# Kernel optimization log

Measured on AMD Instinct MI355X. Metric: run time of the kernel, lower is better.

## Reference

```python
import jax, jax.numpy as jnp
import numpy as np

N_NODES = 50000
N_EDGES = 800000
IN_DIM = 128
OUT_DIM = 128
NUM_RELS = 100
NUM_BASES = 4


def setup_inputs() -> dict:
    key = jax.random.key(0)
    ks = jax.random.split(key, 8)
    h = jax.random.normal(ks[0], (N_NODES, IN_DIM), dtype=jnp.float32)
    norm = jax.random.uniform(ks[1], (N_NODES, 1), dtype=jnp.float32)
    src = jax.random.randint(ks[2], (N_EDGES,), 0, N_NODES, dtype=jnp.int32)
    dst = jax.random.randint(ks[3], (N_EDGES,), 0, N_NODES, dtype=jnp.int32)
    rel_type = jax.random.randint(ks[4], (N_EDGES,), 0, NUM_RELS, dtype=jnp.int32)
    basis_weights = jax.random.normal(ks[5], (NUM_BASES, IN_DIM, OUT_DIM), dtype=jnp.float32) * (2.0 / np.sqrt(IN_DIM + OUT_DIM))
    coefficients = jax.random.normal(ks[6], (NUM_RELS, NUM_BASES), dtype=jnp.float32) * (1.0 / np.sqrt(NUM_RELS + NUM_BASES))
    loop_weight = jax.random.normal(ks[7], (IN_DIM, OUT_DIM), dtype=jnp.float32) * (2.0 / np.sqrt(IN_DIM + OUT_DIM))
    return {
        'h': h, 'norm': norm, 'src': src, 'dst': dst, 'rel_type': rel_type,
        'basis_weights': basis_weights, 'coefficients': coefficients,
        'loop_weight': loop_weight,
    }


def reference(h, norm, src, dst, rel_type, basis_weights, coefficients, loop_weight):
    # h: (N, in), norm: (N, 1), src/dst/rel_type: (E,)
    # basis_weights: (B, in, out), coefficients: (R, B), loop_weight: (in, out)
    n_nodes = h.shape[0]
    num_bases = basis_weights.shape[0]

    # self-loop message (dropout=0 -> identity)
    loop_message = h @ loop_weight  # (N, out)

    # W[r] = sum_b coeff[r, b] * basis[b]; per-edge msg_e = h[src_e] @ W[rel_e].
    # Reassociated: project nodes by each basis once, then mix per edge by
    # the relation coefficients -- identical math, avoids the (E, in, out)
    # gathered weight tensor of the original per-edge bmm.
    hb = jnp.einsum('ni,bio->bno', h, basis_weights)  # (B, N, out)
    c_e = coefficients[rel_type]  # (E, B)
    msg = c_e[:, 0, None] * hb[0][src]
    for b in range(1, num_bases):  # small fixed basis count
        msg = msg + c_e[:, b, None] * hb[b][src]  # (E, out)

    # scatter-sum aggregation to destination nodes, then norm scaling
    agg = jax.ops.segment_sum(msg, dst, num_segments=n_nodes)  # (N, out)
    node_repr = agg * norm  # _apply_func
    node_repr = node_repr + loop_message  # self-loop (bias=None)
    return jax.nn.relu(node_repr)  # activation
```

## Files before the change

kernel.cpp:

```cpp
#include <hip/hip_runtime.h>

typedef short bf16x8 __attribute__((ext_vector_type(8)));
typedef float floatx4 __attribute__((ext_vector_type(4)));
typedef float floatx2 __attribute__((ext_vector_type(2)));

typedef const __attribute__((address_space(1))) void* gas_ptr;
typedef __attribute__((address_space(3))) void* las_ptr;

#define EPB  4096
#define MAXB 6144

__device__ __forceinline__ unsigned short f2bf(float f) {
    unsigned int u = __float_as_uint(f);
    unsigned int r = u + 0x7fffu + ((u >> 16) & 1u);
    return (unsigned short)(r >> 16);
}

__device__ __forceinline__ void stage16(const void* g, void* lbase, int lane) {
#if __has_builtin(__builtin_amdgcn_global_load_lds)
    __builtin_amdgcn_global_load_lds((gas_ptr)g, (las_ptr)lbase, 16, 0, 0);
#else
    *(float4*)((char*)lbase + lane * 16) = *(const float4*)g;
#endif
}

__global__ __launch_bounds__(1024) void prep_all(
    const float* __restrict__ h, unsigned short* __restrict__ hbf, int nconv8,
    const int* __restrict__ dst, int* __restrict__ gh, int E, int nB, int nblkH,
    const float* __restrict__ basis, const float* __restrict__ loopw,
    unsigned short* __restrict__ WT2, int nb_conv)
{
    __shared__ int lh[256];
    const int b = blockIdx.x;
    const int t = threadIdx.x;
    if (b < nb_conv) {
        int idx = b * 1024 + t;
        if (idx < nconv8) {
            const float4 v0 = *(const float4*)(h + (size_t)idx * 8);
            const float4 v1 = *(const float4*)(h + (size_t)idx * 8 + 4);
            uint4 p;
            p.x = (unsigned int)f2bf(v0.x) | ((unsigned int)f2bf(v0.y) << 16);
            p.y = (unsigned int)f2bf(v0.z) | ((unsigned int)f2bf(v0.w) << 16);
            p.z = (unsigned int)f2bf(v1.x) | ((unsigned int)f2bf(v1.y) << 16);
            p.w = (unsigned int)f2bf(v1.z) | ((unsigned int)f2bf(v1.w) << 16);
            *(uint4*)(hbf + (size_t)idx * 8) = p;
        }
    } else if (b < nb_conv + nblkH) {
        const int blk = b - nb_conv;
        if (t < 256) lh[t] = 0;
        __syncthreads();
        const int cbase = blk * EPB;
#pragma unroll
        for (int j = 0; j < EPB / 1024; ++j) {
            int e = cbase + j * 1024 + t;
            if (e < E) atomicAdd(&lh[dst[e] >> 8], 1);
        }
        __syncthreads();
        if (t < nB) gh[(size_t)t * nblkH + blk] = lh[t];
    } else {
        int c = b - nb_conv - nblkH;
        if (t < 640) {
            float v;
            if (t < 512) v = basis[(size_t)t * 128 + c];
            else         v = loopw[(size_t)(t - 512) * 128 + c];
            WT2[(size_t)c * 640 + t] = f2bf(v);
        }
    }
}

__global__ __launch_bounds__(256) void scan1(
    const int* __restrict__ in, int* __restrict__ bsum, int M)
{
    __shared__ int s[256];
    int i = blockIdx.x * 256 + threadIdx.x;
    int t = threadIdx.x;
    s[t] = (i < M) ? in[i] : 0;
    __syncthreads();
    for (int o = 128; o > 0; o >>= 1) {
        if (t < o) s[t] += s[t + o];
        __syncthreads();
    }
    if (t == 0) bsum[blockIdx.x] = s[0];
}

__global__ __launch_bounds__(256) void scan_final(
    const int* __restrict__ in, const int* __restrict__ bsum,
    int* __restrict__ out, int M)
{
    __shared__ int s[256];
    __shared__ int sb[256];
    int t = threadIdx.x;
    int i = blockIdx.x * 256 + t;
    sb[t] = (t < (int)blockIdx.x) ? bsum[t] : 0;
    int v = (i < M) ? in[i] : 0;
    s[t] = v;
    __syncthreads();
    for (int o = 128; o > 0; o >>= 1) {
        if (t < o) sb[t] += sb[t + o];
        __syncthreads();
    }
    for (int o = 1; o < 256; o <<= 1) {
        int x = (t >= o) ? s[t - o] : 0;
        __syncthreads();
        s[t] += x;
        __syncthreads();
    }
    if (i < M) out[i] = s[t] - v + sb[0];
}

__global__ __launch_bounds__(1024) void scatter_bkt(
    const int* __restrict__ dst, const int* __restrict__ src,
    const int* __restrict__ rel, const int* __restrict__ sgh,
    unsigned int* __restrict__ tmp, int E, int nB, int nblkH)
{
    __shared__ int cur[256];
    const int blk = blockIdx.x;
    const int t = threadIdx.x;
    if (t < nB) cur[t] = sgh[(size_t)t * nblkH + blk];
    __syncthreads();
    const int cbase = blk * EPB;
#pragma unroll
    for (int j = 0; j < EPB / 1024; ++j) {
        int e = cbase + j * 1024 + t;
        if (e < E) {
            int d = dst[e];
            int slot = atomicAdd(&cur[d >> 8], 1);
            tmp[slot] = (unsigned int)src[e] | ((unsigned int)rel[e] << 16)
                      | ((unsigned int)(d & 255) << 23);
        }
    }
}

__global__ __launch_bounds__(1024) void bucket_sort(
    const unsigned int* __restrict__ tmp, const int* __restrict__ sgh,
    unsigned int* __restrict__ sedge, int* __restrict__ rowptr,
    int E, int N, int nB, int nblkH)
{
    __shared__ unsigned int eb[MAXB];
    __shared__ int hh[256], ss[256], cur[256];
    const int b = blockIdx.x;
    const int t = threadIdx.x;
    const int brow = sgh[(size_t)b * nblkH];
    const int next = (b + 1 < nB) ? sgh[(size_t)(b + 1) * nblkH] : E;
    int n = next - brow;
    if (n > MAXB) n = MAXB;
    if (t < 256) hh[t] = 0;
    __syncthreads();
    for (int i = t; i < n; i += 1024) {
        unsigned int v = tmp[brow + i];
        eb[i] = v;
        atomicAdd(&hh[(v >> 23) & 255], 1);
    }
    __syncthreads();
    int v = 0;
    if (t < 256) { v = hh[t]; ss[t] = v; }
    __syncthreads();
    for (int o = 1; o < 256; o <<= 1) {
        int x = 0;
        if (t < 256 && t >= o) x = ss[t - o];
        __syncthreads();
        if (t < 256) ss[t] += x;
        __syncthreads();
    }
    if (t < 256) {
        const int excl = ss[t] - v;
        const int idx = b * 256 + t;
        if (idx <= N) rowptr[idx] = brow + excl;
        cur[t] = excl;
    }
    __syncthreads();
    for (int i = t; i < n; i += 1024) {
        unsigned int e = eb[i];
        int slot = atomicAdd(&cur[(e >> 23) & 255], 1);
        sedge[brow + slot] = ((e & 0xFFFFu) << 8) | (((e >> 16) & 0x7Fu) << 25);
    }
}

__global__ __launch_bounds__(256, 8) void aggregate_pre(
    const unsigned short* __restrict__ hbf,
    const int* __restrict__ rowptr,
    const unsigned int* __restrict__ sedge,
    const float* __restrict__ coeff,
    const float* __restrict__ norm,
    unsigned short* __restrict__ A2, int N, int R)
{
    __shared__ float scoef[512];
    for (int i = threadIdx.x; i < R * 4; i += 256) scoef[i] = coeff[i];
    __syncthreads();

    const int wave = threadIdx.x >> 6;
    const int lane = threadIdx.x & 63;
    const int d = blockIdx.x * 4 + wave;
    if (d >= N) return;
    int i = rowptr[d];
    const int end = rowptr[d + 1];

    const char* hbase = (const char*)hbf + lane * 4;

    floatx2 a0 = {0.f, 0.f}, a1 = {0.f, 0.f}, a2 = {0.f, 0.f}, a3 = {0.f, 0.f};

#define EDGE_LOAD(v, u) \
    unsigned int u = *(const unsigned int*)(hbase + ((v) & 0x00FFFF00u));
#define EDGE_MATH(v, u) { \
    const float4 c = *(const float4*)((const char*)scoef + (((v) >> 25) << 4)); \
    floatx2 hp; \
    hp[0] = __uint_as_float((u) << 16); \
    hp[1] = __uint_as_float((u) & 0xFFFF0000u); \
    a0 = __builtin_elementwise_fma((floatx2){c.x, c.x}, hp, a0); \
    a1 = __builtin_elementwise_fma((floatx2){c.y, c.y}, hp, a1); \
    a2 = __builtin_elementwise_fma((floatx2){c.z, c.z}, hp, a2); \
    a3 = __builtin_elementwise_fma((floatx2){c.w, c.w}, hp, a3); }

    while (i < end && (i & 3)) {
        unsigned int v = sedge[i];
        EDGE_LOAD(v, u)
        EDGE_MATH(v, u)
        ++i;
    }
    for (; i + 16 <= end; i += 16) {
        uint4 e0 = *(const uint4*)(sedge + i);
        uint4 e1 = *(const uint4*)(sedge + i + 4);
        uint4 e2 = *(const uint4*)(sedge + i + 8);
        uint4 e3 = *(const uint4*)(sedge + i + 12);
        EDGE_LOAD(e0.x, u0)  EDGE_LOAD(e0.y, u1)  EDGE_LOAD(e0.z, u2)  EDGE_LOAD(e0.w, u3)
        EDGE_LOAD(e1.x, u4)  EDGE_LOAD(e1.y, u5)  EDGE_LOAD(e1.z, u6)  EDGE_LOAD(e1.w, u7)
        EDGE_LOAD(e2.x, u8)  EDGE_LOAD(e2.y, u9)  EDGE_LOAD(e2.z, u10) EDGE_LOAD(e2.w, u11)
        EDGE_LOAD(e3.x, u12) EDGE_LOAD(e3.y, u13) EDGE_LOAD(e3.z, u14) EDGE_LOAD(e3.w, u15)
        EDGE_MATH(e0.x, u0)  EDGE_MATH(e0.y, u1)  EDGE_MATH(e0.z, u2)  EDGE_MATH(e0.w, u3)
        EDGE_MATH(e1.x, u4)  EDGE_MATH(e1.y, u5)  EDGE_MATH(e1.z, u6)  EDGE_MATH(e1.w, u7)
        EDGE_MATH(e2.x, u8)  EDGE_MATH(e2.y, u9)  EDGE_MATH(e2.z, u10) EDGE_MATH(e2.w, u11)
        EDGE_MATH(e3.x, u12) EDGE_MATH(e3.y, u13) EDGE_MATH(e3.z, u14) EDGE_MATH(e3.w, u15)
    }
    for (; i + 8 <= end; i += 8) {
        uint4 e0 = *(const uint4*)(sedge + i);
        uint4 e1 = *(const uint4*)(sedge + i + 4);
        EDGE_LOAD(e0.x, u0) EDGE_LOAD(e0.y, u1) EDGE_LOAD(e0.z, u2) EDGE_LOAD(e0.w, u3)
        EDGE_LOAD(e1.x, u4) EDGE_LOAD(e1.y, u5) EDGE_LOAD(e1.z, u6) EDGE_LOAD(e1.w, u7)
        EDGE_MATH(e0.x, u0) EDGE_MATH(e0.y, u1) EDGE_MATH(e0.z, u2) EDGE_MATH(e0.w, u3)
        EDGE_MATH(e1.x, u4) EDGE_MATH(e1.y, u5) EDGE_MATH(e1.z, u6) EDGE_MATH(e1.w, u7)
    }
    for (; i + 4 <= end; i += 4) {
        uint4 e0 = *(const uint4*)(sedge + i);
        EDGE_LOAD(e0.x, u0) EDGE_LOAD(e0.y, u1) EDGE_LOAD(e0.z, u2) EDGE_LOAD(e0.w, u3)
        EDGE_MATH(e0.x, u0) EDGE_MATH(e0.y, u1) EDGE_MATH(e0.z, u2) EDGE_MATH(e0.w, u3)
    }
    for (; i < end; ++i) {
        unsigned int v = sedge[i];
        EDGE_LOAD(v, u)
        EDGE_MATH(v, u)
    }
#undef EDGE_LOAD
#undef EDGE_MATH

    const float nm = norm[d];
    unsigned short* row = A2 + (size_t)d * 512 + lane * 2;
    *(unsigned int*)(row)       = (unsigned int)f2bf(a0[0] * nm) | ((unsigned int)f2bf(a0[1] * nm) << 16);
    *(unsigned int*)(row + 128) = (unsigned int)f2bf(a1[0] * nm) | ((unsigned int)f2bf(a1[1] * nm) << 16);
    *(unsigned int*)(row + 256) = (unsigned int)f2bf(a2[0] * nm) | ((unsigned int)f2bf(a2[1] * nm) << 16);
    *(unsigned int*)(row + 384) = (unsigned int)f2bf(a3[0] * nm) | ((unsigned int)f2bf(a3[1] * nm) << 16);
}

__global__ __launch_bounds__(256) void final_gemm(
    const unsigned short* __restrict__ A2,
    const unsigned short* __restrict__ hbf,
    const unsigned short* __restrict__ WT2,
    float* __restrict__ out, int N)
{
    __shared__ char sA[16384];
    __shared__ char sB[16384];
    const int t = threadIdx.x;
    const int w = t >> 6;
    const int lane = t & 63;
    const int quad = lane >> 4;
    const int low  = lane & 15;
    const int wr = w >> 1, wc = w & 1;
    const int m0 = blockIdx.x * 128;

    floatx4 acc[4][4];
#pragma unroll
    for (int mt = 0; mt < 4; ++mt)
#pragma unroll
        for (int nt = 0; nt < 4; ++nt) acc[mt][nt] = (floatx4){0.f, 0.f, 0.f, 0.f};

    for (int it = 0; it < 10; ++it) {
        const int k0 = it * 64;
#pragma unroll
        for (int i = 0; i < 4; ++i) {
            const int slot = i * 256 + t;
            const int kc  = slot >> 7;
            const int idx = slot & 127;
            int grow = m0 + idx;
            if (grow >= N) grow = N - 1;
            const unsigned short* gA = (k0 < 512)
                ? A2  + (size_t)grow * 512 + k0 + kc * 8
                : hbf + (size_t)grow * 128 + (k0 - 512) + kc * 8;
            const unsigned short* gB = WT2 + (size_t)idx * 640 + k0 + kc * 8;
            stage16(gA, sA + (size_t)(i * 256 + w * 64) * 16, lane);
            stage16(gB, sB + (size_t)(i * 256 + w * 64) * 16, lane);
        }
        __syncthreads();

#pragma unroll
        for (int ks = 0; ks < 2; ++ks) {
            bf16x8 af[4], bfr[4];
#pragma unroll
            for (int mt = 0; mt < 4; ++mt)
                af[mt] = *(const bf16x8*)(sA + (size_t)(((ks * 4 + quad) << 7) + wr * 64 + mt * 16 + low) * 16);
#pragma unroll
            for (int nt = 0; nt < 4; ++nt)
                bfr[nt] = *(const bf16x8*)(sB + (size_t)(((ks * 4 + quad) << 7) + wc * 64 + nt * 16 + low) * 16);
#pragma unroll
            for (int mt = 0; mt < 4; ++mt)
#pragma unroll
                for (int nt = 0; nt < 4; ++nt)
                    acc[mt][nt] = __builtin_amdgcn_mfma_f32_16x16x32_bf16(af[mt], bfr[nt], acc[mt][nt], 0, 0, 0);
        }
        __syncthreads();
    }

#pragma unroll
    for (int mt = 0; mt < 4; ++mt) {
#pragma unroll
        for (int nt = 0; nt < 4; ++nt) {
            const int c = wc * 64 + nt * 16 + low;
#pragma unroll
            for (int r = 0; r < 4; ++r) {
                int rr = m0 + wr * 64 + mt * 16 + quad * 4 + r;
                if (rr < N) out[(size_t)rr * 128 + c] = fmaxf(acc[mt][nt][r], 0.f);
            }
        }
    }
}

extern "C" void kernel_launch(void* const* d_in, const int* in_sizes, int n_in,
                              void* d_out, int out_size, void* d_ws, size_t ws_size,
                              hipStream_t stream)
{
    const float* h     = (const float*)d_in[0];
    const float* norm  = (const float*)d_in[1];
    const int*   src   = (const int*)d_in[2];
    const int*   dst   = (const int*)d_in[3];
    const int*   rel   = (const int*)d_in[4];
    const float* basis = (const float*)d_in[5];
    const float* coeff = (const float*)d_in[6];
    const float* loopw = (const float*)d_in[7];
    float* out = (float*)d_out;

    const int N = in_sizes[1];
    const int E = in_sizes[2];
    const int R = in_sizes[6] / 4;

    const int nB    = (N + 255) >> 8;
    const int nblkH = (E + EPB - 1) / EPB;
    const int M     = nB * nblkH;
    const int NBs   = (M + 255) / 256;

    char* ws = (char*)d_ws;
    size_t off = 0;
    auto walloc = [&](size_t bytes) -> char* {
        char* p = ws + off;
        off = (off + bytes + 255) & ~(size_t)255;
        return p;
    };
    unsigned short* A2     = (unsigned short*)walloc((size_t)N * 512 * 2);
    unsigned short* hbf    = (unsigned short*)walloc((size_t)N * 128 * 2);
    unsigned short* WT2    = (unsigned short*)walloc(128 * 640 * 2);
    int*            rowptr = (int*)walloc((size_t)(N + 1) * 4);
    int*            bsum   = (int*)walloc((size_t)NBs * 4);
    int*            gh     = (int*)walloc((size_t)M * 4);
    int*            sgh    = (int*)walloc((size_t)M * 4);
    unsigned int*   tmp    = (unsigned int*)walloc((size_t)E * 4);
    unsigned int*   sedge  = (unsigned int*)walloc((size_t)E * 4);

    const int nconv8  = N * 16;
    const int nb_conv = (nconv8 + 1023) / 1024;

    prep_all<<<nb_conv + nblkH + 128, 1024, 0, stream>>>(
        h, hbf, nconv8, dst, gh, E, nB, nblkH, basis, loopw, WT2, nb_conv);
    scan1<<<NBs, 256, 0, stream>>>(gh, bsum, M);
    scan_final<<<NBs, 256, 0, stream>>>(gh, bsum, sgh, M);
    scatter_bkt<<<nblkH, 1024, 0, stream>>>(dst, src, rel, sgh, tmp, E, nB, nblkH);
    bucket_sort<<<nB, 1024, 0, stream>>>(tmp, sgh, sedge, rowptr, E, N, nB, nblkH);
    aggregate_pre<<<(N + 3) / 4, 256, 0, stream>>>(hbf, rowptr, sedge, coeff, norm, A2, N, R);
    final_gemm<<<(N + 127) / 128, 256, 0, stream>>>(A2, hbf, WT2, out, N);
}
```

Baseline: 189.9 us.

## Fuse edge bucketing into prep kernel using global atomic bucket reservations

```diff
diff --git a/kernel.cpp b/kernel.cpp
--- a/kernel.cpp
+++ b/kernel.cpp
@@ -26,11 +26,13 @@
 
 __global__ __launch_bounds__(1024) void prep_all(
     const float* __restrict__ h, unsigned short* __restrict__ hbf, int nconv8,
-    const int* __restrict__ dst, int* __restrict__ gh, int E, int nB, int nblkH,
+    const int* __restrict__ dst, const int* __restrict__ src,
+    const int* __restrict__ rel, int* __restrict__ bcnt,
+    unsigned int* __restrict__ tmp, int E, int nB, int nblkH,
     const float* __restrict__ basis, const float* __restrict__ loopw,
     unsigned short* __restrict__ WT2, int nb_conv)
 {
-    __shared__ int lh[256];
+    __shared__ int lh[256], cur[256];
     const int b = blockIdx.x;
     const int t = threadIdx.x;
     if (b < nb_conv) {
@@ -50,13 +52,33 @@
         if (t < 256) lh[t] = 0;
         __syncthreads();
         const int cbase = blk * EPB;
+        int dd[EPB / 1024];
 #pragma unroll
         for (int j = 0; j < EPB / 1024; ++j) {
             int e = cbase + j * 1024 + t;
-            if (e < E) atomicAdd(&lh[dst[e] >> 8], 1);
-        }
-        __syncthreads();
-        if (t < nB) gh[(size_t)t * nblkH + blk] = lh[t];
+            dd[j] = (e < E) ? dst[e] : -1;
+            if (dd[j] >= 0) atomicAdd(&lh[dd[j] >> 8], 1);
+        }
+        __syncthreads();
+        if (t < 256) {
+            int c = lh[t];
+            int base = c ? atomicAdd(&bcnt[t * 16], c) : 0;
+            cur[t] = t * MAXB + base;
+        }
+        __syncthreads();
+#pragma unroll
+        for (int j = 0; j < EPB / 1024; ++j) {
+            int e = cbase + j * 1024 + t;
+            int d = dd[j];
+            if (d >= 0) {
+                int bin = d >> 8;
+                int slot = atomicAdd(&cur[bin], 1);
+                if (slot < (bin + 1) * MAXB)
+                    tmp[slot] = (unsigned int)src[e]
+                              | ((unsigned int)rel[e] << 16)
+                              | ((unsigned int)(d & 255) << 23);
+            }
+        }
     } else {
         int c = b - nb_conv - nblkH;
         if (t < 640) {
@@ -68,86 +90,41 @@
     }
 }
 
-__global__ __launch_bounds__(256) void scan1(
-    const int* __restrict__ in, int* __restrict__ bsum, int M)
-{
-    __shared__ int s[256];
-    int i = blockIdx.x * 256 + threadIdx.x;
-    int t = threadIdx.x;
-    s[t] = (i < M) ? in[i] : 0;
-    __syncthreads();
-    for (int o = 128; o > 0; o >>= 1) {
-        if (t < o) s[t] += s[t + o];
-        __syncthreads();
-    }
-    if (t == 0) bsum[blockIdx.x] = s[0];
-}
-
-__global__ __launch_bounds__(256) void scan_final(
-    const int* __restrict__ in, const int* __restrict__ bsum,
-    int* __restrict__ out, int M)
-{
-    __shared__ int s[256];
-    __shared__ int sb[256];
-    int t = threadIdx.x;
-    int i = blockIdx.x * 256 + t;
-    sb[t] = (t < (int)blockIdx.x) ? bsum[t] : 0;
-    int v = (i < M) ? in[i] : 0;
-    s[t] = v;
-    __syncthreads();
-    for (int o = 128; o > 0; o >>= 1) {
-        if (t < o) sb[t] += sb[t + o];
-        __syncthreads();
-    }
-    for (int o = 1; o < 256; o <<= 1) {
-        int x = (t >= o) ? s[t - o] : 0;
-        __syncthreads();
-        s[t] += x;
-        __syncthreads();
-    }
-    if (i < M) out[i] = s[t] - v + sb[0];
-}
-
-__global__ __launch_bounds__(1024) void scatter_bkt(
-    const int* __restrict__ dst, const int* __restrict__ src,
-    const int* __restrict__ rel, const int* __restrict__ sgh,
-    unsigned int* __restrict__ tmp, int E, int nB, int nblkH)
-{
-    __shared__ int cur[256];
-    const int blk = blockIdx.x;
-    const int t = threadIdx.x;
-    if (t < nB) cur[t] = sgh[(size_t)t * nblkH + blk];
-    __syncthreads();
-    const int cbase = blk * EPB;
-#pragma unroll
-    for (int j = 0; j < EPB / 1024; ++j) {
-        int e = cbase + j * 1024 + t;
-        if (e < E) {
-            int d = dst[e];
-            int slot = atomicAdd(&cur[d >> 8], 1);
-            tmp[slot] = (unsigned int)src[e] | ((unsigned int)rel[e] << 16)
-                      | ((unsigned int)(d & 255) << 23);
-        }
-    }
-}
-
 __global__ __launch_bounds__(1024) void bucket_sort(
-    const unsigned int* __restrict__ tmp, const int* __restrict__ sgh,
+    const unsigned int* __restrict__ tmp, const int* __restrict__ bcnt,
     unsigned int* __restrict__ sedge, int* __restrict__ rowptr,
-    int E, int N, int nB, int nblkH)
+    int E, int N, int nB)
 {
     __shared__ unsigned int eb[MAXB];
     __shared__ int hh[256], ss[256], cur[256];
+    __shared__ int sbrow, scnt;
     const int b = blockIdx.x;
     const int t = threadIdx.x;
-    const int brow = sgh[(size_t)b * nblkH];
-    const int next = (b + 1 < nB) ? sgh[(size_t)(b + 1) * nblkH] : E;
-    int n = next - brow;
-    if (n > MAXB) n = MAXB;
+
+    int c = 0;
+    if (t < 256) {
+        c = (t < nB) ? bcnt[t * 16] : 0;
+        if (c > MAXB) c = MAXB;
+        ss[t] = c;
+    }
+    __syncthreads();
+    for (int o = 1; o < 256; o <<= 1) {
+        int x = 0;
+        if (t < 256 && t >= o) x = ss[t - o];
+        __syncthreads();
+        if (t < 256) ss[t] += x;
+        __syncthreads();
+    }
+    if (t == b) { sbrow = ss[t] - c; scnt = c; }
+    __syncthreads();
+    const int brow = sbrow;
+    const int n    = scnt;
+
     if (t < 256) hh[t] = 0;
     __syncthreads();
+    const unsigned int* tb = tmp + (size_t)b * MAXB;
     for (int i = t; i < n; i += 1024) {
-        unsigned int v = tmp[brow + i];
+        unsigned int v = tb[i];
         eb[i] = v;
         atomicAdd(&hh[(v >> 23) & 255], 1);
     }
@@ -352,8 +329,6 @@
 
     const int nB    = (N + 255) >> 8;
     const int nblkH = (E + EPB - 1) / EPB;
-    const int M     = nB * nblkH;
-    const int NBs   = (M + 255) / 256;
 
     char* ws = (char*)d_ws;
     size_t off = 0;
@@ -366,21 +341,18 @@
     unsigned short* hbf    = (unsigned short*)walloc((size_t)N * 128 * 2);
     unsigned short* WT2    = (unsigned short*)walloc(128 * 640 * 2);
     int*            rowptr = (int*)walloc((size_t)(N + 1) * 4);
-    int*            bsum   = (int*)walloc((size_t)NBs * 4);
-    int*            gh     = (int*)walloc((size_t)M * 4);
-    int*            sgh    = (int*)walloc((size_t)M * 4);
-    unsigned int*   tmp    = (unsigned int*)walloc((size_t)E * 4);
+    int*            bcnt   = (int*)walloc((size_t)nB * 16 * 4);
+    unsigned int*   tmp    = (unsigned int*)walloc((size_t)nB * MAXB * 4);
     unsigned int*   sedge  = (unsigned int*)walloc((size_t)E * 4);
 
     const int nconv8  = N * 16;
     const int nb_conv = (nconv8 + 1023) / 1024;
 
+    hipMemsetAsync(bcnt, 0, (size_t)nB * 16 * 4, stream);
     prep_all<<<nb_conv + nblkH + 128, 1024, 0, stream>>>(
-        h, hbf, nconv8, dst, gh, E, nB, nblkH, basis, loopw, WT2, nb_conv);
-    scan1<<<NBs, 256, 0, stream>>>(gh, bsum, M);
-    scan_final<<<NBs, 256, 0, stream>>>(gh, bsum, sgh, M);
-    scatter_bkt<<<nblkH, 1024, 0, stream>>>(dst, src, rel, sgh, tmp, E, nB, nblkH);
-    bucket_sort<<<nB, 1024, 0, stream>>>(tmp, sgh, sedge, rowptr, E, N, nB, nblkH);
+        h, hbf, nconv8, dst, src, rel, bcnt, tmp, E, nB, nblkH,
+        basis, loopw, WT2, nb_conv);
+    bucket_sort<<<nB, 1024, 0, stream>>>(tmp, bcnt, sedge, rowptr, E, N, nB);
     aggregate_pre<<<(N + 3) / 4, 256, 0, stream>>>(hbf, rowptr, sedge, coeff, norm, A2, N, R);
     final_gemm<<<(N + 127) / 128, 256, 0, stream>>>(A2, hbf, WT2, out, N);
 }
```

Result: no change. 187.4 us (-1.3%).
